# Kernel tuning notes

Measured on AMD Instinct MI355X. Metric: run time of the kernel, lower is better.

## Reference

```python
import jax, jax.numpy as jnp
import numpy as np

TEMP = 0.07
LN_EPS = 1e-5


def _l2norm(x, eps=1e-12):
    n = jnp.linalg.norm(x, axis=-1, keepdims=True)
    return x / jnp.maximum(n, eps)


def setup_inputs() -> dict:
    key = jax.random.key(0)
    ks = jax.random.split(key, 8)
    B, N, D, S = 1024, 100000, 1024, 2
    scale = 1.0 / np.sqrt(D)
    return {
        "q": jax.random.normal(ks[0], (B, D), jnp.float32),
        "bank_values": jax.random.normal(ks[1], (N, D), jnp.float32),
        "proj_w": jax.random.normal(ks[2], (S, D, D), jnp.float32) * scale,
        "proj_b": jax.random.normal(ks[3], (S, D), jnp.float32) * 0.01,
        "unify_w": jax.random.normal(ks[4], (S, D, D), jnp.float32) * scale,
        "unify_b": jax.random.normal(ks[5], (S, D), jnp.float32) * 0.01,
        "ln_gamma": jnp.ones((D,), jnp.float32),
        "ln_beta": jnp.zeros((D,), jnp.float32),
        "top_m": 32,
    }


def reference(q, bank_values, proj_w, proj_b, unify_w, unify_b, ln_gamma, ln_beta, top_m):
    # PrototypeBank.build: keys = L2-normalized values (detached)
    keys = _l2norm(bank_values)  # [N, D]
    num_scales = proj_w.shape[0]
    ref = jnp.zeros_like(q)
    for s in range(num_scales):  # small fixed structural loop
        p = q @ proj_w[s].T + proj_b[s]                       # [B, D] Linear
        scores = _l2norm(p) @ keys.T                          # [B, N] cosine
        top_s, top_i = jax.lax.top_k(scores, top_m)           # [B, m]
        attn = jax.nn.softmax(top_s / TEMP, axis=-1)          # [B, m]
        z = jnp.einsum('bm,bmd->bd', attn, bank_values[top_i])  # weighted gather-sum
        ref = ref + z @ unify_w[s].T + unify_b[s]
    mu = ref.mean(axis=-1, keepdims=True)
    var = ref.var(axis=-1, keepdims=True)
    out = (ref - mu) * jax.lax.rsqrt(var + LN_EPS) * ln_gamma + ln_beta
    return out
```

## Files before the change

kernel.cpp:

```cpp
#include <hip/hip_runtime.h>
#include <math.h>


static inline size_t align256(size_t x){ return (x + 255) & ~size_t(255); }

typedef short bf16x8 __attribute__((ext_vector_type(8)));
typedef float f32x4  __attribute__((ext_vector_type(4)));

#define GLOAD_LDS16(gp, lp) \
  __builtin_amdgcn_global_load_lds((const __attribute__((address_space(1))) unsigned int*)(gp), \
                                   (__attribute__((address_space(3))) unsigned int*)(lp), 16, 0, 0)

__device__ inline unsigned short f2bf(float f){
  unsigned int u = __float_as_uint(f);
  u += 0x7fffu + ((u >> 16) & 1u);
  return (unsigned short)(u >> 16);
}
__device__ inline float bf2f(unsigned int h16){
  return __uint_as_float(h16 << 16);
}

__global__ __launch_bounds__(256) void row_rnorm_kernel(
    const float* __restrict__ X, float* __restrict__ rn, int rows, int D)
{
  int wv = threadIdx.x >> 6, lane = threadIdx.x & 63;
  int r = blockIdx.x * 4 + wv;
  if (r >= rows) return;
  const float4* xr = (const float4*)(X + (size_t)r * D);
  int nv = D >> 2;
  float ss = 0.f;
  for (int i = lane; i < nv; i += 64){
    float4 v = xr[i];
    ss = fmaf(v.x,v.x, fmaf(v.y,v.y, fmaf(v.z,v.z, fmaf(v.w,v.w, ss))));
  }
  #pragma unroll
  for (int off = 32; off; off >>= 1) ss += __shfl_xor(ss, off);
  if (lane == 0) rn[r] = 1.f / fmaxf(sqrtf(ss), 1e-12f);
}

__global__ __launch_bounds__(256) void convert_bf16_kernel(
    const float* __restrict__ X, const float* __restrict__ rowscale,
    unsigned short* __restrict__ out, long total8, int D)
{
  long i = (long)blockIdx.x * 256 + threadIdx.x;
  const long stride = (long)gridDim.x * 256;
  for (; i < total8; i += stride){
    long e = i * 8;
    int r = (int)(e / D);
    float sc = rowscale ? rowscale[r] : 1.f;
    float4 v0 = *(const float4*)(X + e);
    float4 v1 = *(const float4*)(X + e + 4);
    v0.x*=sc; v0.y*=sc; v0.z*=sc; v0.w*=sc;
    v1.x*=sc; v1.y*=sc; v1.z*=sc; v1.w*=sc;
    uint4 w;
    w.x = (unsigned)f2bf(v0.x) | ((unsigned)f2bf(v0.y) << 16);
    w.y = (unsigned)f2bf(v0.z) | ((unsigned)f2bf(v0.w) << 16);
    w.z = (unsigned)f2bf(v1.x) | ((unsigned)f2bf(v1.y) << 16);
    w.w = (unsigned)f2bf(v1.z) | ((unsigned)f2bf(v1.w) << 16);
    *(uint4*)(out + e) = w;
  }
}

template<int RM, int RN, bool ACCUM>
__global__ __launch_bounds__(256) void gemm_nt_kernel(
    const float* __restrict__ A, const float* __restrict__ B,
    const float* __restrict__ bias, const float* __restrict__ bscale,
    float* __restrict__ C, int M, int Nn, int K, int Brows, int ldc)
{
  __shared__ float As[16][RM*64 + 4];
  __shared__ float Bs[16][RN*64 + 4];
  const int t  = threadIdx.x;
  const int tm = t >> 4, tn = t & 15;
  const int m0 = blockIdx.y * (RM*64), n0 = blockIdx.x * (RN*64);

  float acc[RM][RN][4][4];
  #pragma unroll
  for (int r=0;r<RM;++r)
    #pragma unroll
    for (int c=0;c<RN;++c)
      #pragma unroll
      for (int i=0;i<4;++i)
        #pragma unroll
        for (int j=0;j<4;++j) acc[r][c][i][j]=0.f;

  for (int kp = 0; kp < K; kp += 16){
    #pragma unroll
    for (int l = 0; l < RM; ++l){
      int li = t + l*256;
      int row = li >> 2, kq = (li & 3) << 2;
      float4 v = *(const float4*)(A + (size_t)(m0+row)*K + kp + kq);
      As[kq+0][row]=v.x; As[kq+1][row]=v.y; As[kq+2][row]=v.z; As[kq+3][row]=v.w;
    }
    #pragma unroll
    for (int l = 0; l < RN; ++l){
      int li = t + l*256;
      int row = li >> 2, kq = (li & 3) << 2;
      int gn = n0 + row;
      float4 v = make_float4(0.f,0.f,0.f,0.f);
      float sc = 1.f;
      if (gn < Brows){
        v = *(const float4*)(B + (size_t)gn*K + kp + kq);
        if (bscale) sc = bscale[gn];
      }
      Bs[kq+0][row]=v.x*sc; Bs[kq+1][row]=v.y*sc; Bs[kq+2][row]=v.z*sc; Bs[kq+3][row]=v.w*sc;
    }
    __syncthreads();
    #pragma unroll
    for (int kk = 0; kk < 16; ++kk){
      float av[RM][4], bv[RN][4];
      #pragma unroll
      for (int r=0;r<RM;++r){
        float4 a = *(const float4*)&As[kk][r*64 + tm*4];
        av[r][0]=a.x; av[r][1]=a.y; av[r][2]=a.z; av[r][3]=a.w;
      }
      #pragma unroll
      for (int c=0;c<RN;++c){
        float4 b = *(const float4*)&Bs[kk][c*64 + tn*4];
        bv[c][0]=b.x; bv[c][1]=b.y; bv[c][2]=b.z; bv[c][3]=b.w;
      }
      #pragma unroll
      for (int r=0;r<RM;++r)
        #pragma unroll
        for (int c=0;c<RN;++c)
          #pragma unroll
          for (int i=0;i<4;++i)
            #pragma unroll
            for (int j=0;j<4;++j)
              acc[r][c][i][j] = fmaf(av[r][i], bv[c][j], acc[r][c][i][j]);
    }
    __syncthreads();
  }

  #pragma unroll
  for (int r=0;r<RM;++r){
    #pragma unroll
    for (int i=0;i<4;++i){
      int gm = m0 + r*64 + tm*4 + i;
      #pragma unroll
      for (int c=0;c<RN;++c){
        int gn = n0 + c*64 + tn*4;
        if (gn >= Nn) continue;
        float* cp = C + (size_t)gm*ldc + gn;
        float o0=acc[r][c][i][0], o1=acc[r][c][i][1], o2=acc[r][c][i][2], o3=acc[r][c][i][3];
        if (gn + 3 < Nn){
          float4 o = make_float4(o0,o1,o2,o3);
          if (bias){ float4 bb = *(const float4*)&bias[gn]; o.x+=bb.x; o.y+=bb.y; o.z+=bb.z; o.w+=bb.w; }
          if (ACCUM){ float4 cc = *(const float4*)cp; o.x+=cc.x; o.y+=cc.y; o.z+=cc.z; o.w+=cc.w; }
          *(float4*)cp = o;
        } else {
          float ov[4] = {o0,o1,o2,o3};
          for (int j=0;j<4;++j){
            if (gn + j < Nn){
              float o = ov[j];
              if (bias)  o += bias[gn+j];
              if (ACCUM) o += cp[j];
              cp[j] = o;
            }
          }
        }
      }
    }
  }
}

__global__ __launch_bounds__(512, 2) void scores_mfma_kernel(
    const unsigned short* __restrict__ Abf, const unsigned short* __restrict__ Bbf,
    unsigned short* __restrict__ C, int M, int Nn, int K, int ldc)
{
  __shared__ __align__(16) unsigned char smem[65536];

  const int t = threadIdx.x;
  const int lane = t & 63, wid = t >> 6;
  const int wm = wid >> 2, wn = wid & 3;
  const int l15 = lane & 15, l4 = lane >> 4;
  const int m0 = blockIdx.y * 256, n0 = blockIdx.x * 256;

  f32x4 acc[8][4];
  #pragma unroll
  for (int i=0;i<8;++i)
    #pragma unroll
    for (int j=0;j<4;++j) acc[i][j] = (f32x4)0.f;

  const int srow = t >> 2;
  const int sb   = (t & 3) * 16;
  const int ldsb = wid * 1024;

  const int NT = K >> 5;

  #define STAGE(kp, bufsel)                                                   \
    {                                                                         \
      unsigned char* Ab_ = smem + (bufsel)*32768;                             \
      unsigned char* Bb_ = smem + (bufsel)*32768 + 16384;                     \
      _Pragma("unroll")                                                       \
      for (int i_ = 0; i_ < 2; ++i_){                                         \
        int row_ = srow + i_*128;                                             \
        int src_ = sb ^ ((row_ & 3) << 4);                                    \
        const unsigned char* ga_ = (const unsigned char*)Abf                  \
            + ((size_t)(m0+row_)*K + (kp))*2 + src_;                          \
        GLOAD_LDS16(ga_, Ab_ + ldsb + i_*8192);                               \
        int gn_ = n0 + row_; if (gn_ >= Nn) gn_ = Nn - 1;                     \
        const unsigned char* gb_ = (const unsigned char*)Bbf                  \
            + ((size_t)gn_*K + (kp))*2 + src_;                                \
        GLOAD_LDS16(gb_, Bb_ + ldsb + i_*8192);                               \
      }                                                                       \
    }

  STAGE(0, 0);
  __syncthreads();

  int cur = 0;
  for (int tt = 0; tt < NT; ++tt){
    if (tt + 1 < NT) STAGE((tt+1) << 5, cur ^ 1);

    const unsigned char* Ab = smem + cur*32768;
    const unsigned char* Bb = smem + cur*32768 + 16384;

    bf16x8 Bf[4];
    #pragma unroll
    for (int fn = 0; fn < 4; ++fn){
      int br = wn*64 + fn*16 + l15;
      Bf[fn] = *(const bf16x8*)(Bb + br*64 + ((l4*16) ^ ((br & 3) << 4)));
    }
    #pragma unroll
    for (int fm = 0; fm < 8; ++fm){
      int ar = wm*128 + fm*16 + l15;
      bf16x8 Af = *(const bf16x8*)(Ab + ar*64 + ((l4*16) ^ ((ar & 3) << 4)));
      #pragma unroll
      for (int fn = 0; fn < 4; ++fn)
        acc[fm][fn] = __builtin_amdgcn_mfma_f32_16x16x32_bf16(Af, Bf[fn], acc[fm][fn], 0,0,0);
    }
    __syncthreads();
    cur ^= 1;
  }
  #undef STAGE

  #pragma unroll
  for (int fm = 0; fm < 8; ++fm){
    int row = m0 + wm*128 + fm*16 + l4*4;
    #pragma unroll
    for (int fn = 0; fn < 4; ++fn){
      int col = n0 + wn*64 + fn*16 + l15;
      if (col < Nn){
        unsigned short* cp = C + (size_t)row*ldc + col;
        #pragma unroll
        for (int r = 0; r < 4; ++r) cp[(size_t)r*ldc] = f2bf(acc[fm][fn][r]);
      }
    }
  }
}

__global__ __launch_bounds__(256) void chunk_filter_kernel(
    const unsigned short* __restrict__ scores, int ldc, int colbase, int Nwindow,
    int NC, float* __restrict__ cand_s, int* __restrict__ cand_i,
    int chunk0, int nchunks_total, int cap, float eps)
{
  extern __shared__ float lds[];
  __shared__ float sv[256];
  __shared__ float tau_s;
  __shared__ int cnt;
  const int row = blockIdx.x, t = threadIdx.x;
  const int lc = blockIdx.y;
  const int col0l = lc * NC;
  int ncols = Nwindow - col0l; if (ncols > NC) ncols = NC;
  const int gchunk = chunk0 + lc;
  const unsigned short* sr = scores + (size_t)row * ldc + col0l;

  float m0 = -INFINITY, m1 = -INFINITY, m2 = -INFINITY, m3 = -INFINITY;
  const int nc8 = ncols >> 3;
  const uint4* sr8 = (const uint4*)sr;
  float4* lds4 = (float4*)lds;
  for (int j = t; j < nc8; j += 256){
    uint4 v = sr8[j];
    float4 a = make_float4(bf2f(v.x & 0xffffu), bf2f(v.x >> 16),
                           bf2f(v.y & 0xffffu), bf2f(v.y >> 16));
    float4 b = make_float4(bf2f(v.z & 0xffffu), bf2f(v.z >> 16),
                           bf2f(v.w & 0xffffu), bf2f(v.w >> 16));
    lds4[j*2]   = a;
    lds4[j*2+1] = b;
    m0 = fmaxf(m0, fmaxf(a.x, b.x)); m1 = fmaxf(m1, fmaxf(a.y, b.y));
    m2 = fmaxf(m2, fmaxf(a.z, b.z)); m3 = fmaxf(m3, fmaxf(a.w, b.w));
  }
  for (int j = (nc8 << 3) + t; j < ncols; j += 256){
    float v = bf2f((unsigned)sr[j]);
    lds[j] = v;
    m0 = fmaxf(m0, v);
  }
  sv[t] = fmaxf(fmaxf(m0, m1), fmaxf(m2, m3));
  __syncthreads();

  for (int k = 2; k <= 256; k <<= 1){
    for (int j = k >> 1; j > 0; j >>= 1){
      int p = t ^ j;
      float a = sv[t], b = sv[p];
      bool up = ((t & k) == 0);
      float keep = (t < p) ? (up ? fmaxf(a,b) : fminf(a,b))
                           : (up ? fminf(a,b) : fmaxf(a,b));
      __syncthreads();
      sv[t] = keep;
      __syncthreads();
    }
  }
  if (t == 0){ tau_s = sv[31]; cnt = 0; }
  __syncthreads();
  const float thr = tau_s - eps;

  float* cs = cand_s + ((size_t)row * nchunks_total + gchunk) * cap;
  int*   ci = cand_i + ((size_t)row * nchunks_total + gchunk) * cap;

  for (int j = t; j < ncols; j += 256){
    float v = lds[j];
    if (v >= thr){
      int pos = atomicAdd(&cnt, 1);
      if (pos < cap){ cs[pos] = v; ci[pos] = colbase + col0l + j; }
    }
  }
  __syncthreads();
  int n = cnt < cap ? cnt : cap;
  for (int j = n + t; j < cap; j += 256) ci[j] = -1;
}

__global__ __launch_bounds__(256) void select_softmax_gather_kernel(
    const float* __restrict__ cand_s, const int* __restrict__ cand_i,
    const float* __restrict__ p, const float* __restrict__ rn_bank,
    const float* __restrict__ pnorm, const float* __restrict__ bank,
    float* __restrict__ z, int ncap, int D, int topm, float invtemp, float eps)
{
  __shared__ float p_s[1024];
  __shared__ float vs[1024]; __shared__ int vi[1024];
  __shared__ float sv[256];
  __shared__ int   cidx[256];
  __shared__ float rv[256];
  __shared__ float tau_s;
  __shared__ int cnt;
  const int row = blockIdx.x, t = threadIdx.x;
  const int lane = t & 63, wid = t >> 6;

  const float4* pr = (const float4*)(p + (size_t)row * D);
  for (int i = t; i < (D >> 2); i += 256) ((float4*)p_s)[i] = pr[i];
  const float* cs = cand_s + (size_t)row * ncap;
  const int*  ci = cand_i + (size_t)row * ncap;
  for (int j = t; j < ncap; j += 256){
    int k = ci[j];
    vi[j] = k;
    vs[j] = (k >= 0) ? cs[j] : -INFINITY;
  }
  __syncthreads();

  float m = -INFINITY;
  for (int j = t; j < ncap; j += 256) m = fmaxf(m, vs[j]);
  sv[t] = m;
  __syncthreads();
  for (int k = 2; k <= 256; k <<= 1){
    for (int j = k >> 1; j > 0; j >>= 1){
      int pp = t ^ j;
      float a = sv[t], b = sv[pp];
      bool up = ((t & k) == 0);
      float keep = (t < pp) ? (up ? fmaxf(a,b) : fminf(a,b))
                            : (up ? fminf(a,b) : fmaxf(a,b));
      __syncthreads();
      sv[t] = keep;
      __syncthreads();
    }
  }
  if (t == 0){ tau_s = sv[31]; cnt = 0; }
  __syncthreads();
  const float thr = tau_s - eps;

  for (int j = t; j < ncap; j += 256){
    if (vi[j] >= 0 && vs[j] >= thr){
      int pos = atomicAdd(&cnt, 1);
      if (pos < 256) cidx[pos] = vi[j];
    }
  }
  __syncthreads();
  const int n2 = cnt < 256 ? cnt : 256;
  rv[t] = -INFINITY;
  if (t >= n2) cidx[t] = 0x7fffffff;
  __syncthreads();

  const int nj = D >> 8;
  for (int c = wid; c < n2; c += 4){
    int idx = cidx[c];
    const float4* kr = (const float4*)(bank + (size_t)idx * D);
    float ss = 0.f;
    for (int j = 0; j < nj; ++j){
      float4 kv = kr[lane + j*64];
      float4 pv = *(const float4*)&p_s[(lane + j*64) << 2];
      ss = fmaf(pv.x,kv.x, fmaf(pv.y,kv.y, fmaf(pv.z,kv.z, fmaf(pv.w,kv.w, ss))));
    }
    #pragma unroll
    for (int off = 32; off; off >>= 1) ss += __shfl_xor(ss, off);
    if (lane == 0) rv[c] = ss * rn_bank[idx];
  }
  __syncthreads();

  for (int k = 2; k <= 256; k <<= 1){
    for (int j = k >> 1; j > 0; j >>= 1){
      int pp = t ^ j;
      float av = rv[t];  int ai = cidx[t];
      float bv = rv[pp]; int bi = cidx[pp];
      bool up = ((t & k) == 0);
      bool agtb = (av > bv) || (av == bv && ai < bi);
      bool keepA = (t < pp) ? (up ? agtb : !agtb)
                            : (up ? !agtb : agtb);
      __syncthreads();
      if (keepA){ rv[t] = av; cidx[t] = ai; } else { rv[t] = bv; cidx[t] = bi; }
      __syncthreads();
    }
  }

  if (t == 0){
    float pn = pnorm[row] * invtemp;
    float mx = rv[0] * pn;
    float sum = 0.f;
    for (int i = 0; i < topm; ++i){
      float w = expf(rv[i]*pn - mx);
      sv[i] = w; sum += w;
    }
    float inv = 1.f / sum;
    for (int i = 0; i < topm; ++i) sv[i] *= inv;
  }
  __syncthreads();

  for (int d4 = t; d4 < (D >> 2); d4 += 256){
    float ax=0.f, ay=0.f, az=0.f, aw=0.f;
    for (int i = 0; i < topm; ++i){
      float a = sv[i];
      const float4 v = *(const float4*)(bank + (size_t)cidx[i]*D + (d4<<2));
      ax = fmaf(a, v.x, ax); ay = fmaf(a, v.y, ay);
      az = fmaf(a, v.z, az); aw = fmaf(a, v.w, aw);
    }
    *(float4*)(z + (size_t)row*D + (d4<<2)) = make_float4(ax,ay,az,aw);
  }
}

__global__ __launch_bounds__(256) void layernorm_kernel(
    const float* __restrict__ ref, const float* __restrict__ gamma,
    const float* __restrict__ beta, float* __restrict__ out, int D, float eps)
{
  __shared__ float s1[4], s2[4];
  const int row = blockIdx.x, t = threadIdx.x;
  const float4* xr = (const float4*)(ref + (size_t)row*D);
  int nv = D >> 2;
  float sum = 0.f, ssq = 0.f;
  for (int i = t; i < nv; i += 256){
    float4 v = xr[i];
    sum += v.x+v.y+v.z+v.w;
    ssq = fmaf(v.x,v.x, fmaf(v.y,v.y, fmaf(v.z,v.z, fmaf(v.w,v.w, ssq))));
  }
  const int lane = t & 63, wid = t >> 6;
  #pragma unroll
  for (int off = 32; off; off >>= 1){ sum += __shfl_xor(sum, off); ssq += __shfl_xor(ssq, off); }
  if (lane == 0){ s1[wid] = sum; s2[wid] = ssq; }
  __syncthreads();
  sum = s1[0]+s1[1]+s1[2]+s1[3];
  ssq = s2[0]+s2[1]+s2[2]+s2[3];
  float mu  = sum / (float)D;
  float var = ssq / (float)D - mu*mu;
  float rs  = rsqrtf(var + eps);
  const float4* g4 = (const float4*)gamma;
  const float4* b4 = (const float4*)beta;
  float4* o4 = (float4*)(out + (size_t)row*D);
  for (int i = t; i < nv; i += 256){
    float4 v = xr[i], g = g4[i], bb = b4[i];
    float4 o;
    o.x = (v.x-mu)*rs*g.x + bb.x;
    o.y = (v.y-mu)*rs*g.y + bb.y;
    o.z = (v.z-mu)*rs*g.z + bb.z;
    o.w = (v.w-mu)*rs*g.w + bb.w;
    o4[i] = o;
  }
}

extern "C" void kernel_launch(void* const* d_in, const int* in_sizes, int n_in,
                              void* d_out, int out_size, void* d_ws, size_t ws_size,
                              hipStream_t stream)
{
  const float* q       = (const float*)d_in[0];
  const float* bank    = (const float*)d_in[1];
  const float* proj_w  = (const float*)d_in[2];
  const float* proj_b  = (const float*)d_in[3];
  const float* unify_w = (const float*)d_in[4];
  const float* unify_b = (const float*)d_in[5];
  const float* gamma   = (const float*)d_in[6];
  const float* beta    = (const float*)d_in[7];

  const int D = in_sizes[6];
  const int B = in_sizes[0] / D;
  const int N = in_sizes[1] / D;
  const int S = in_sizes[2] / (D * D);
  const int TOPM = 32;
  const int CAP  = 64;
  const int NC   = 12544;
  const int WCH  = 4;
  const float INVTEMP = 1.0f / 0.07f;
  const float EPS = 0.025f;

  const int NCH = (N + NC - 1) / NC;
  const int SCW = NC * WCH;

  char* wsb = (char*)d_ws;
  size_t off = 0;
  auto take = [&](size_t bytes)->char*{ char* p = wsb + off; off += align256(bytes); return p; };
  float* rn_bank = (float*)take((size_t)N*4);
  float* pnorm   = (float*)take((size_t)B*4);
  float* p       = (float*)take((size_t)B*D*4);
  float* z       = (float*)take((size_t)B*D*4);
  float* ref     = (float*)take((size_t)B*D*4);
  float* cand_s  = (float*)take((size_t)B*NCH*CAP*4);
  int*   cand_i  = (int*)  take((size_t)B*NCH*CAP*4);
  unsigned short* bank_bf = (unsigned short*)take((size_t)N*D*2);
  unsigned short* p_bf    = (unsigned short*)take((size_t)B*D*2);
  unsigned short* scores  = (unsigned short*)take((size_t)B*(size_t)SCW*2);

  row_rnorm_kernel<<<(N+3)/4, 256, 0, stream>>>(bank, rn_bank, N, D);
  convert_bf16_kernel<<<2048, 256, 0, stream>>>(
      bank, rn_bank, bank_bf, (long)N*D/8, D);

  for (int s = 0; s < S; ++s){
    dim3 g1(D/64, B/64);
    gemm_nt_kernel<1,1,false><<<g1, 256, 0, stream>>>(
        q, proj_w + (size_t)s*D*D, proj_b + (size_t)s*D, nullptr,
        p, B, D, D, D, D);
    row_rnorm_kernel<<<(B+3)/4, 256, 0, stream>>>(p, pnorm, B, D);
    convert_bf16_kernel<<<512, 256, 0, stream>>>(
        p, nullptr, p_bf, (long)B*D/8, D);

    for (int w0 = 0; w0 < N; w0 += SCW){
      int nw = N - w0; if (nw > SCW) nw = SCW;
      dim3 g2((nw + 255)/256, B/256);
      scores_mfma_kernel<<<g2, 512, 0, stream>>>(
          p_bf, bank_bf + (size_t)w0*D,
          scores, B, nw, D, SCW);
      int ncw = (nw + NC - 1) / NC;
      chunk_filter_kernel<<<dim3(B, ncw), 256, (size_t)NC*4, stream>>>(
          scores, SCW, w0, nw, NC, cand_s, cand_i,
          w0 / NC, NCH, CAP, EPS);
    }

    select_softmax_gather_kernel<<<B, 256, 0, stream>>>(
        cand_s, cand_i, p, rn_bank, pnorm, bank, z,
        NCH*CAP, D, TOPM, INVTEMP, EPS);

    if (s == 0)
      gemm_nt_kernel<1,1,false><<<g1, 256, 0, stream>>>(
          z, unify_w + (size_t)s*D*D, unify_b + (size_t)s*D, nullptr,
          ref, B, D, D, D, D);
    else
      gemm_nt_kernel<1,1,true><<<g1, 256, 0, stream>>>(
          z, unify_w + (size_t)s*D*D, unify_b + (size_t)s*D, nullptr,
          ref, B, D, D, D, D);
  }

  layernorm_kernel<<<B, 256, 0, stream>>>(ref, gamma, beta, (float*)d_out, D, 1e-5f);
}
```

Measured before the change: 1.501 ms.

## Batch both scales into one scores pass and shrink MFMA tile to 128x128

Stacks the projected queries of both scales into a single R=S*B row matrix, so the bank scan (scores GEMM plus chunk filter) and the gather run once over twice the rows instead of once per scale. The bank is then streamed from memory once rather than twice. At the same time the scores kernel moves from 256x256 double-buffered tiles with 512 threads to 128x128 single-buffered tiles with 256 threads. That loses the load/compute overlap and lowers per-block data reuse, and the scores and candidate buffers double in size.

Measured after the change: 1.529 ms. No clear change (+1.9%).

```diff
diff --git a/kernel.cpp b/kernel.cpp
--- a/kernel.cpp
+++ b/kernel.cpp
@@ -163,21 +163,21 @@
   }
 }
 
-__global__ __launch_bounds__(512, 2) void scores_mfma_kernel(
+__global__ __launch_bounds__(256) void scores_mfma_kernel(
     const unsigned short* __restrict__ Abf, const unsigned short* __restrict__ Bbf,
     unsigned short* __restrict__ C, int M, int Nn, int K, int ldc)
 {
-  __shared__ __align__(16) unsigned char smem[65536];
+  __shared__ __align__(16) unsigned char smem[16384];
 
   const int t = threadIdx.x;
   const int lane = t & 63, wid = t >> 6;
-  const int wm = wid >> 2, wn = wid & 3;
+  const int wm = wid >> 1, wn = wid & 1;
   const int l15 = lane & 15, l4 = lane >> 4;
-  const int m0 = blockIdx.y * 256, n0 = blockIdx.x * 256;
-
-  f32x4 acc[8][4];
+  const int m0 = blockIdx.y * 128, n0 = blockIdx.x * 128;
+
+  f32x4 acc[4][4];
   #pragma unroll
-  for (int i=0;i<8;++i)
+  for (int i=0;i<4;++i)
     #pragma unroll
     for (int j=0;j<4;++j) acc[i][j] = (f32x4)0.f;
 
@@ -185,58 +185,43 @@
   const int sb   = (t & 3) * 16;
   const int ldsb = wid * 1024;
 
-  const int NT = K >> 5;
-
-  #define STAGE(kp, bufsel)                                                   \
-    {                                                                         \
-      unsigned char* Ab_ = smem + (bufsel)*32768;                             \
-      unsigned char* Bb_ = smem + (bufsel)*32768 + 16384;                     \
-      _Pragma("unroll")                                                       \
-      for (int i_ = 0; i_ < 2; ++i_){                                         \
-        int row_ = srow + i_*128;                                             \
-        int src_ = sb ^ ((row_ & 3) << 4);                                    \
-        const unsigned char* ga_ = (const unsigned char*)Abf                  \
-            + ((size_t)(m0+row_)*K + (kp))*2 + src_;                          \
-        GLOAD_LDS16(ga_, Ab_ + ldsb + i_*8192);                               \
-        int gn_ = n0 + row_; if (gn_ >= Nn) gn_ = Nn - 1;                     \
-        const unsigned char* gb_ = (const unsigned char*)Bbf                  \
-            + ((size_t)gn_*K + (kp))*2 + src_;                                \
-        GLOAD_LDS16(gb_, Bb_ + ldsb + i_*8192);                               \
-      }                                                                       \
-    }
-
-  STAGE(0, 0);
-  __syncthreads();
-
-  int cur = 0;
-  for (int tt = 0; tt < NT; ++tt){
-    if (tt + 1 < NT) STAGE((tt+1) << 5, cur ^ 1);
-
-    const unsigned char* Ab = smem + cur*32768;
-    const unsigned char* Bb = smem + cur*32768 + 16384;
-
+  for (int kp = 0; kp < K; kp += 32){
+    #pragma unroll
+    for (int i = 0; i < 2; ++i){
+      int row = srow + i*64;
+      int src = sb ^ ((row & 3) << 4);
+      const unsigned char* ga = (const unsigned char*)Abf
+          + ((size_t)(m0+row)*K + kp)*2 + src;
+      GLOAD_LDS16(ga, smem + i*4096 + ldsb);
+      int gn = n0 + row; if (gn >= Nn) gn = Nn - 1;
+      const unsigned char* gb = (const unsigned char*)Bbf
+          + ((size_t)gn*K + kp)*2 + src;
+      GLOAD_LDS16(gb, smem + 8192 + i*4096 + ldsb);
+    }
+    __syncthreads();
+
+    const unsigned char* As_ = smem;
+    const unsigned char* Bs_ = smem + 8192;
     bf16x8 Bf[4];
     #pragma unroll
     for (int fn = 0; fn < 4; ++fn){
       int br = wn*64 + fn*16 + l15;
-      Bf[fn] = *(const bf16x8*)(Bb + br*64 + ((l4*16) ^ ((br & 3) << 4)));
-    }
-    #pragma unroll
-    for (int fm = 0; fm < 8; ++fm){
-      int ar = wm*128 + fm*16 + l15;
-      bf16x8 Af = *(const bf16x8*)(Ab + ar*64 + ((l4*16) ^ ((ar & 3) << 4)));
+      Bf[fn] = *(const bf16x8*)(Bs_ + br*64 + ((l4*16) ^ ((br & 3) << 4)));
+    }
+    #pragma unroll
+    for (int fm = 0; fm < 4; ++fm){
+      int ar = wm*64 + fm*16 + l15;
+      bf16x8 Af = *(const bf16x8*)(As_ + ar*64 + ((l4*16) ^ ((ar & 3) << 4)));
       #pragma unroll
       for (int fn = 0; fn < 4; ++fn)
         acc[fm][fn] = __builtin_amdgcn_mfma_f32_16x16x32_bf16(Af, Bf[fn], acc[fm][fn], 0,0,0);
     }
     __syncthreads();
-    cur ^= 1;
-  }
-  #undef STAGE
+  }
 
   #pragma unroll
-  for (int fm = 0; fm < 8; ++fm){
-    int row = m0 + wm*128 + fm*16 + l4*4;
+  for (int fm = 0; fm < 4; ++fm){
+    int row = m0 + wm*64 + fm*16 + l4*4;
     #pragma unroll
     for (int fn = 0; fn < 4; ++fn){
       int col = n0 + wn*64 + fn*16 + l15;
@@ -489,6 +474,7 @@
   const int B = in_sizes[0] / D;
   const int N = in_sizes[1] / D;
   const int S = in_sizes[2] / (D * D);
+  const int R = S * B;
   const int TOPM = 32;
   const int CAP  = 64;
   const int NC   = 12544;
@@ -503,52 +489,54 @@
   size_t off = 0;
   auto take = [&](size_t bytes)->char*{ char* p = wsb + off; off += align256(bytes); return p; };
   float* rn_bank = (float*)take((size_t)N*4);
-  float* pnorm   = (float*)take((size_t)B*4);
-  float* p       = (float*)take((size_t)B*D*4);
-  float* z       = (float*)take((size_t)B*D*4);
+  float* pnorm   = (float*)take((size_t)R*4);
+  float* p       = (float*)take((size_t)R*D*4);
+  float* z       = (float*)take((size_t)R*D*4);
   float* ref     = (float*)take((size_t)B*D*4);
-  float* cand_s  = (float*)take((size_t)B*NCH*CAP*4);
-  int*   cand_i  = (int*)  take((size_t)B*NCH*CAP*4);
+  float* cand_s  = (float*)take((size_t)R*NCH*CAP*4);
+  int*   cand_i  = (int*)  take((size_t)R*NCH*CAP*4);
   unsigned short* bank_bf = (unsigned short*)take((size_t)N*D*2);
-  unsigned short* p_bf    = (unsigned short*)take((size_t)B*D*2);
-  unsigned short* scores  = (unsigned short*)take((size_t)B*(size_t)SCW*2);
+  unsigned short* p_bf    = (unsigned short*)take((size_t)R*D*2);
+  unsigned short* scores  = (unsigned short*)take((size_t)R*(size_t)SCW*2);
 
   row_rnorm_kernel<<<(N+3)/4, 256, 0, stream>>>(bank, rn_bank, N, D);
   convert_bf16_kernel<<<2048, 256, 0, stream>>>(
       bank, rn_bank, bank_bf, (long)N*D/8, D);
 
-  for (int s = 0; s < S; ++s){
-    dim3 g1(D/64, B/64);
+  dim3 g1(D/64, B/64);
+  for (int s = 0; s < S; ++s)
     gemm_nt_kernel<1,1,false><<<g1, 256, 0, stream>>>(
         q, proj_w + (size_t)s*D*D, proj_b + (size_t)s*D, nullptr,
-        p, B, D, D, D, D);
-    row_rnorm_kernel<<<(B+3)/4, 256, 0, stream>>>(p, pnorm, B, D);
-    convert_bf16_kernel<<<512, 256, 0, stream>>>(
-        p, nullptr, p_bf, (long)B*D/8, D);
-
-    for (int w0 = 0; w0 < N; w0 += SCW){
-      int nw = N - w0; if (nw > SCW) nw = SCW;
-      dim3 g2((nw + 255)/256, B/256);
-      scores_mfma_kernel<<<g2, 512, 0, stream>>>(
-          p_bf, bank_bf + (size_t)w0*D,
-          scores, B, nw, D, SCW);
-      int ncw = (nw + NC - 1) / NC;
-      chunk_filter_kernel<<<dim3(B, ncw), 256, (size_t)NC*4, stream>>>(
-          scores, SCW, w0, nw, NC, cand_s, cand_i,
-          w0 / NC, NCH, CAP, EPS);
-    }
-
-    select_softmax_gather_kernel<<<B, 256, 0, stream>>>(
-        cand_s, cand_i, p, rn_bank, pnorm, bank, z,
-        NCH*CAP, D, TOPM, INVTEMP, EPS);
-
+        p + (size_t)s*B*D, B, D, D, D, D);
+
+  row_rnorm_kernel<<<(R+3)/4, 256, 0, stream>>>(p, pnorm, R, D);
+  convert_bf16_kernel<<<1024, 256, 0, stream>>>(
+      p, nullptr, p_bf, (long)R*D/8, D);
+
+  for (int w0 = 0; w0 < N; w0 += SCW){
+    int nw = N - w0; if (nw > SCW) nw = SCW;
+    dim3 g2((nw + 127)/128, R/128);
+    scores_mfma_kernel<<<g2, 256, 0, stream>>>(
+        p_bf, bank_bf + (size_t)w0*D,
+        scores, R, nw, D, SCW);
+    int ncw = (nw + NC - 1) / NC;
+    chunk_filter_kernel<<<dim3(R, ncw), 256, (size_t)NC*4, stream>>>(
+        scores, SCW, w0, nw, NC, cand_s, cand_i,
+        w0 / NC, NCH, CAP, EPS);
+  }
+
+  select_softmax_gather_kernel<<<R, 256, 0, stream>>>(
+      cand_s, cand_i, p, rn_bank, pnorm, bank, z,
+      NCH*CAP, D, TOPM, INVTEMP, EPS);
+
+  for (int s = 0; s < S; ++s){
     if (s == 0)
       gemm_nt_kernel<1,1,false><<<g1, 256, 0, stream>>>(
-          z, unify_w + (size_t)s*D*D, unify_b + (size_t)s*D, nullptr,
+          z + (size_t)s*B*D, unify_w + (size_t)s*D*D, unify_b + (size_t)s*D, nullptr,
           ref, B, D, D, D, D);
     else
       gemm_nt_kernel<1,1,true><<<g1, 256, 0, stream>>>(
-          z, unify_w + (size_t)s*D*D, unify_b + (size_t)s*D, nullptr,
+          z + (size_t)s*B*D, unify_w + (size_t)s*D*D, unify_b + (size_t)s*D, nullptr,
           ref, B, D, D, D, D);
   }
 
```
